# Kernel tuning notes

Measured on AMD Instinct MI355X. Metric: run time of the kernel, lower is better.

Reference implementation:

```python
import jax, jax.numpy as jnp
import numpy as np

GRID = 8        # kornia equalize_clahe default grid_size=(8,8)
NUM_BINS = 256  # kornia default
CLIP_LIMIT = 40.0


def normalize_in_range(x, lo, hi):
    mn, mx = x.min(), x.max()
    return (x - mn) / (mx - mn) * (hi - lo) + lo


def equalize_clahe(x, clip_limit=CLIP_LIMIT, grid=GRID, bins=NUM_BINS):
    # x: (B, C, H, W) in [0, 1]; H, W divisible by grid
    B, C, H, W = x.shape
    th, tw = H // grid, W // grid
    pixels = th * tw

    # --- per-pixel bin index (histc with bins=256, min=0, max=1) ---
    bidx = jnp.clip((x * bins).astype(jnp.int32), 0, bins - 1)  # (B,C,H,W)

    # --- per-tile histograms via one segment_sum (scatter-add) ---
    ti = (jnp.arange(H) // th)[None, None, :, None]
    tj = (jnp.arange(W) // tw)[None, None, None, :]
    bb = jnp.arange(B)[:, None, None, None]
    cc = jnp.arange(C)[None, :, None, None]
    tile_id = ((bb * C + cc) * grid + ti) * grid + tj          # (B,C,H,W)
    flat = (tile_id * bins + bidx).reshape(-1)
    hist = jax.ops.segment_sum(
        jnp.ones(flat.shape, jnp.float32), flat,
        num_segments=B * C * grid * grid * bins,
    ).reshape(B, C, grid, grid, bins)

    # --- clip histogram and redistribute excess uniformly ---
    max_val = max(int(clip_limit * pixels // bins), 1)
    hist = jnp.minimum(hist, max_val)
    residual = (pixels - hist.sum(-1, keepdims=True)) / bins
    hist = hist + residual

    # --- CDF -> LUT (values in [0, bins-1], floored) ---
    lut = jnp.floor(jnp.clip(jnp.cumsum(hist, axis=-1) * ((bins - 1) / pixels),
                             0.0, bins - 1.0))                 # (B,C,gh,gw,bins)

    # --- bilinear interpolation between the 4 nearest tile LUTs ---
    gi = jnp.clip((jnp.arange(H) + 0.5) / th - 0.5, 0.0, grid - 1.0)
    gj = jnp.clip((jnp.arange(W) + 0.5) / tw - 0.5, 0.0, grid - 1.0)
    i0 = jnp.floor(gi).astype(jnp.int32); i1 = jnp.minimum(i0 + 1, grid - 1)
    j0 = jnp.floor(gj).astype(jnp.int32); j1 = jnp.minimum(j0 + 1, grid - 1)
    wy = (gi - i0)[None, None, :, None]
    wx = (gj - j0)[None, None, None, :]

    I0 = i0[None, None, :, None]; I1 = i1[None, None, :, None]
    J0 = j0[None, None, None, :]; J1 = j1[None, None, None, :]

    v00 = lut[bb, cc, I0, J0, bidx]
    v01 = lut[bb, cc, I0, J1, bidx]
    v10 = lut[bb, cc, I1, J0, bidx]
    v11 = lut[bb, cc, I1, J1, bidx]

    out = (1.0 - wy) * ((1.0 - wx) * v00 + wx * v01) + wy * ((1.0 - wx) * v10 + wx * v11)
    return out / (bins - 1)


def setup_inputs() -> dict:
    key = jax.random.key(0)
    kx, ky = jax.random.split(key)
    x = jax.random.normal(kx, (16, 1, 1024, 1024), dtype=jnp.float32)
    y = jax.random.randint(ky, (16,), 0, 10, dtype=jnp.int64)
    return {"x": x, "y": y}


def reference(x, y):
    x = normalize_in_range(x, 0.0, 1.0)
    mean = x.mean(axis=(0, 2, 3))
    std = jnp.std(x, axis=(0, 2, 3), ddof=1)  # torch unbiased std
    x = (x - mean[None, :, None, None]) / std[None, :, None, None]
    x = normalize_in_range(x, 0.0, 1.0)
    x = equalize_clahe(x, clip_limit=40.0)
    return (x, y)
```

## Files before the change

kernel.cpp:

```cpp
#include <hip/hip_runtime.h>


#define BINS 256
#define FBINS 2048
#define MAXV 2560u

__global__ __launch_bounds__(256, 4) void k_tilestat(const float* __restrict__ x,
                                                     float2* __restrict__ partials,
                                                     unsigned* __restrict__ finehg){
  __shared__ unsigned fh[FBINS];
  __shared__ float smin[4], smax[4];
  __shared__ float sp[2];
  int t = threadIdx.x;
  int tile = blockIdx.x;
  int bc = tile >> 6, ti = (tile >> 3) & 7, tj = tile & 7;
  const float4* x4 = (const float4*)(x + ((size_t)bc * 1024 + ti * 128) * 1024 + tj * 128);
  float4 v[16];
  #pragma unroll
  for (int k = 0; k < 16; k++){
    int p = t + (k << 8);
    v[k] = x4[(p >> 5) * 256 + (p & 31)];
  }
  #pragma unroll
  for (int i = 0; i < FBINS / 256; i++) fh[t + i * 256] = 0u;
  float lmin = INFINITY, lmax = -INFINITY;
  #pragma unroll
  for (int k = 0; k < 16; k++){
    lmin = fminf(lmin, fminf(fminf(v[k].x, v[k].y), fminf(v[k].z, v[k].w)));
    lmax = fmaxf(lmax, fmaxf(fmaxf(v[k].x, v[k].y), fmaxf(v[k].z, v[k].w)));
  }
  for (int o = 32; o > 0; o >>= 1){
    lmin = fminf(lmin, __shfl_down(lmin, o, 64));
    lmax = fmaxf(lmax, __shfl_down(lmax, o, 64));
  }
  int lane = t & 63, wv = t >> 6;
  if (lane == 0){ smin[wv] = lmin; smax[wv] = lmax; }
  __syncthreads();
  if (t == 0){
    float m = smin[0], M = smax[0];
    #pragma unroll
    for (int i = 1; i < 4; i++){ m = fminf(m, smin[i]); M = fmaxf(M, smax[i]); }
    partials[tile] = make_float2(m, M);
    sp[0] = m;
    sp[1] = (float)FBINS / fmaxf(M - m, 1e-30f);
  }
  __syncthreads();
  float tmn = sp[0], tinv = sp[1];
  #pragma unroll
  for (int k = 0; k < 16; k++){
    int b0 = min((int)((v[k].x - tmn) * tinv), FBINS - 1);
    int b1 = min((int)((v[k].y - tmn) * tinv), FBINS - 1);
    int b2 = min((int)((v[k].z - tmn) * tinv), FBINS - 1);
    int b3 = min((int)((v[k].w - tmn) * tinv), FBINS - 1);
    atomicAdd(&fh[b0], 1u);
    atomicAdd(&fh[b1], 1u);
    atomicAdd(&fh[b2], 1u);
    atomicAdd(&fh[b3], 1u);
  }
  __syncthreads();
  unsigned* outp = finehg + (size_t)tile * (FBINS / 2);
  #pragma unroll
  for (int i = 0; i < FBINS / 512; i++){
    int w = t + i * 256;
    outp[w] = (fh[2 * w] & 0xFFFFu) | (fh[2 * w + 1] << 16);
  }
}

__global__ __launch_bounds__(256) void k_lut(const float2* __restrict__ partials,
                                             int nparts,
                                             const unsigned* __restrict__ finehg,
                                             float* __restrict__ lut,
                                             float2* __restrict__ gmm,
                                             const int* __restrict__ y,
                                             float* __restrict__ out,
                                             int N, int tail){
  __shared__ unsigned ch[BINS];
  __shared__ unsigned sc[BINS];
  __shared__ unsigned wsum[4];
  __shared__ float smin[4], smax[4];
  __shared__ float sp[2];
  int t = threadIdx.x;
  int tile = blockIdx.x;
  ch[t] = 0u;
  float lmin = INFINITY, lmax = -INFINITY;
  for (int i = t; i < nparts; i += 256){
    float2 p = partials[i];
    lmin = fminf(lmin, p.x);
    lmax = fmaxf(lmax, p.y);
  }
  for (int o = 32; o > 0; o >>= 1){
    lmin = fminf(lmin, __shfl_down(lmin, o, 64));
    lmax = fmaxf(lmax, __shfl_down(lmax, o, 64));
  }
  int lane = t & 63, wv = t >> 6;
  if (lane == 0){ smin[wv] = lmin; smax[wv] = lmax; }
  __syncthreads();
  if (t == 0){
    float m = smin[0], M = smax[0];
    #pragma unroll
    for (int i = 1; i < 4; i++){ m = fminf(m, smin[i]); M = fmaxf(M, smax[i]); }
    sp[0] = m;
    sp[1] = 1.0f / (M - m);
  }
  __syncthreads();
  float mn = sp[0], inv = sp[1];
  float2 tp = partials[tile];
  float tw = (tp.y - tp.x) * (1.0f / (float)FBINS);
  const unsigned* fhp = finehg + (size_t)tile * (FBINS / 2);
  #pragma unroll
  for (int i = 0; i < 4; i++){
    int w = t + i * 256;
    unsigned pk = fhp[w];
    unsigned c0 = pk & 0xFFFFu, c1 = pk >> 16;
    int f0 = 2 * w;
    if (c0){
      float ctr = tp.x + ((float)f0 + 0.5f) * tw;
      int cb = min(max((int)(((ctr - mn) * inv) * 256.0f), 0), 255);
      atomicAdd(&ch[cb], c0);
    }
    if (c1){
      float ctr = tp.x + ((float)f0 + 1.5f) * tw;
      int cb = min(max((int)(((ctr - mn) * inv) * 256.0f), 0), 255);
      atomicAdd(&ch[cb], c1);
    }
  }
  __syncthreads();
  unsigned h = ch[t];
  if (h > MAXV) h = MAXV;
  unsigned s = h;
  for (int o = 32; o > 0; o >>= 1) s += __shfl_down(s, o, 64);
  if (lane == 0) wsum[wv] = s;
  __syncthreads();
  unsigned total = wsum[0] + wsum[1] + wsum[2] + wsum[3];
  float residual = (16384.0f - (float)total) * (1.0f / 256.0f);
  sc[t] = h;
  __syncthreads();
  for (int o = 1; o < 256; o <<= 1){
    unsigned pv = (t >= o) ? sc[t - o] : 0u;
    __syncthreads();
    sc[t] += pv;
    __syncthreads();
  }
  float cum = ((float)sc[t] + (float)(t + 1) * residual) * (255.0f / 16384.0f);
  lut[(size_t)tile * BINS + t] = floorf(fminf(fmaxf(cum, 0.0f), 255.0f));
  if (tile == 0){
    if (t == 0) *gmm = make_float2(mn, inv);
    if (t < tail) out[N + t] = (float)y[t];
  }
}

__global__ __launch_bounds__(256) void k_apply(const float* __restrict__ x,
                                               const float2* __restrict__ gmm,
                                               const float* __restrict__ lutg,
                                               float* __restrict__ out){
  __shared__ float2 lint[2048];
  int t = threadIdx.x;
  int strip = blockIdx.x;
  int b = strip >> 7;
  int r0 = (strip & 127) << 3;
  float gi = fminf(fmaxf((r0 + 0.5f) * (1.0f / 128.0f) - 0.5f, 0.0f), 7.0f);
  int i0 = (int)gi;
  int i1 = min(i0 + 1, 7);
  const float* g0 = lutg + ((size_t)b * 8 + i0) * 2048;
  const float* g1 = lutg + ((size_t)b * 8 + i1) * 2048;
  #pragma unroll
  for (int i = 0; i < 8; i++){
    int k = t + i * 256;
    lint[k] = make_float2(g0[k], g1[k]);
  }
  float2 mmv = *gmm;
  float mn = mmv.x, inv = mmv.y;
  int j0[4], j1[4];
  float wx[4];
  #pragma unroll
  for (int c = 0; c < 4; c++){
    int col = (t << 2) + c;
    float gj = fminf(fmaxf((col + 0.5f) * (1.0f / 128.0f) - 0.5f, 0.0f), 7.0f);
    j0[c] = (int)gj;
    j1[c] = min(j0[c] + 1, 7);
    wx[c] = gj - (float)j0[c];
  }
  size_t base4 = ((size_t)b * 1024 + r0) * 256;
  __syncthreads();
  #pragma unroll
  for (int r = 0; r < 8; r++){
    int h = r0 + r;
    float giw = fminf(fmaxf((h + 0.5f) * (1.0f / 128.0f) - 0.5f, 0.0f), 7.0f);
    float wy = giw - (float)i0;
    float4 xv = ((const float4*)x)[base4 + r * 256 + t];
    int bi[4];
    bi[0] = min(max((int)(((xv.x - mn) * inv) * 256.0f), 0), 255);
    bi[1] = min(max((int)(((xv.y - mn) * inv) * 256.0f), 0), 255);
    bi[2] = min(max((int)(((xv.z - mn) * inv) * 256.0f), 0), 255);
    bi[3] = min(max((int)(((xv.w - mn) * inv) * 256.0f), 0), 255);
    float res[4];
    #pragma unroll
    for (int c = 0; c < 4; c++){
      float2 p0 = lint[(j0[c] << 8) + bi[c]];
      float2 p1 = lint[(j1[c] << 8) + bi[c]];
      float top = p0.x + wx[c] * (p1.x - p0.x);
      float bot = p0.y + wx[c] * (p1.y - p0.y);
      res[c] = (top + wy * (bot - top)) * (1.0f / 255.0f);
    }
    ((float4*)out)[base4 + r * 256 + t] = make_float4(res[0], res[1], res[2], res[3]);
  }
}

extern "C" void kernel_launch(void* const* d_in, const int* in_sizes, int n_in,
                              void* d_out, int out_size, void* d_ws, size_t ws_size,
                              hipStream_t stream){
  const float* x = (const float*)d_in[0];
  const int* y = (const int*)d_in[1];
  float* out = (float*)d_out;
  int N = in_sizes[0];
  int B = N >> 20;
  int T = B * 64;
  float2* partials = (float2*)d_ws;
  float2* gmm = (float2*)((char*)d_ws + 8192);
  unsigned* fineh = (unsigned*)((char*)d_ws + 16384);
  float* lut = (float*)((char*)d_ws + 16384 + (size_t)T * (FBINS * 2));
  int tail = out_size - N;

  hipLaunchKernelGGL(k_tilestat, dim3(T), dim3(256), 0, stream, x, partials, fineh);
  hipLaunchKernelGGL(k_lut, dim3(T), dim3(256), 0, stream,
                     partials, T, fineh, lut, gmm, y, out, N, tail);
  hipLaunchKernelGGL(k_apply, dim3(B * 128), dim3(256), 0, stream,
                     x, gmm, lut, out);
}
```

Baseline: 131.6 us.

## Fuse tile stats and LUT build into one cooperative kernel with grid sync

Merges the tile min/max pass and the LUT construction into a single cooperative kernel. Each block keeps its tile in registers, a grid-wide sync publishes the global min/max, and the block then bins directly into the final 256-bin histogram. This drops the fine 2048-bin histogram round trip through global memory and one kernel launch. The block scan is also changed to wavefront shuffles. In exchange it depends on all 1024 blocks being co-resident for the cooperative launch, and falls back to the old two-kernel path if that launch fails.

```diff
diff --git a/kernel.cpp b/kernel.cpp
--- a/kernel.cpp
+++ b/kernel.cpp
@@ -1,9 +1,112 @@
 #include <hip/hip_runtime.h>
+#include <hip/hip_cooperative_groups.h>
+
+namespace cg = cooperative_groups;
 
 
 #define BINS 256
 #define FBINS 2048
 #define MAXV 2560u
+
+__global__ __launch_bounds__(256, 4) void k_histlut(const float* __restrict__ x,
+                                                    float2* __restrict__ partials,
+                                                    float* __restrict__ lut,
+                                                    float2* __restrict__ gmm,
+                                                    const int* __restrict__ y,
+                                                    float* __restrict__ out,
+                                                    int N, int tail, int nparts){
+  __shared__ unsigned ch[BINS];
+  __shared__ float smin[4], smax[4];
+  __shared__ float sp[2];
+  __shared__ unsigned wsum[4];
+  int t = threadIdx.x;
+  int tile = blockIdx.x;
+  int bc = tile >> 6, ti = (tile >> 3) & 7, tj = tile & 7;
+  const float4* x4 = (const float4*)(x + ((size_t)bc * 1024 + ti * 128) * 1024 + tj * 128);
+  float4 v[16];
+  #pragma unroll
+  for (int k = 0; k < 16; k++){
+    int p = t + (k << 8);
+    v[k] = x4[(p >> 5) * 256 + (p & 31)];
+  }
+  ch[t] = 0u;
+  float lmin = INFINITY, lmax = -INFINITY;
+  #pragma unroll
+  for (int k = 0; k < 16; k++){
+    lmin = fminf(lmin, fminf(fminf(v[k].x, v[k].y), fminf(v[k].z, v[k].w)));
+    lmax = fmaxf(lmax, fmaxf(fmaxf(v[k].x, v[k].y), fmaxf(v[k].z, v[k].w)));
+  }
+  for (int o = 32; o > 0; o >>= 1){
+    lmin = fminf(lmin, __shfl_down(lmin, o, 64));
+    lmax = fmaxf(lmax, __shfl_down(lmax, o, 64));
+  }
+  int lane = t & 63, wv = t >> 6;
+  if (lane == 0){ smin[wv] = lmin; smax[wv] = lmax; }
+  __syncthreads();
+  if (t == 0){
+    float m = smin[0], M = smax[0];
+    #pragma unroll
+    for (int i = 1; i < 4; i++){ m = fminf(m, smin[i]); M = fmaxf(M, smax[i]); }
+    partials[tile] = make_float2(m, M);
+    __threadfence();
+  }
+  cg::this_grid().sync();
+  float gmn = INFINITY, gmx = -INFINITY;
+  for (int i = t; i < nparts; i += 256){
+    float2 p = partials[i];
+    gmn = fminf(gmn, p.x);
+    gmx = fmaxf(gmx, p.y);
+  }
+  for (int o = 32; o > 0; o >>= 1){
+    gmn = fminf(gmn, __shfl_down(gmn, o, 64));
+    gmx = fmaxf(gmx, __shfl_down(gmx, o, 64));
+  }
+  if (lane == 0){ smin[wv] = gmn; smax[wv] = gmx; }
+  __syncthreads();
+  if (t == 0){
+    float m = smin[0], M = smax[0];
+    #pragma unroll
+    for (int i = 1; i < 4; i++){ m = fminf(m, smin[i]); M = fmaxf(M, smax[i]); }
+    sp[0] = m;
+    sp[1] = 1.0f / (M - m);
+  }
+  __syncthreads();
+  float mn = sp[0], inv = sp[1];
+  #pragma unroll
+  for (int k = 0; k < 16; k++){
+    int b0 = min(max((int)(((v[k].x - mn) * inv) * 256.0f), 0), 255);
+    int b1 = min(max((int)(((v[k].y - mn) * inv) * 256.0f), 0), 255);
+    int b2 = min(max((int)(((v[k].z - mn) * inv) * 256.0f), 0), 255);
+    int b3 = min(max((int)(((v[k].w - mn) * inv) * 256.0f), 0), 255);
+    atomicAdd(&ch[b0], 1u);
+    atomicAdd(&ch[b1], 1u);
+    atomicAdd(&ch[b2], 1u);
+    atomicAdd(&ch[b3], 1u);
+  }
+  __syncthreads();
+  unsigned h = ch[t];
+  if (h > MAXV) h = MAXV;
+  unsigned s = h;
+  #pragma unroll
+  for (int o = 1; o < 64; o <<= 1){
+    unsigned nb = __shfl_up(s, o, 64);
+    if (lane >= o) s += nb;
+  }
+  if (lane == 63) wsum[wv] = s;
+  __syncthreads();
+  unsigned off = 0;
+  #pragma unroll
+  for (int i = 0; i < 3; i++) if (i < wv) off += wsum[i];
+  unsigned total = wsum[0] + wsum[1] + wsum[2] + wsum[3];
+  float residual = (16384.0f - (float)total) * (1.0f / 256.0f);
+  float cum = ((float)(s + off) + (float)(t + 1) * residual) * (255.0f / 16384.0f);
+  lut[(size_t)tile * BINS + t] = floorf(fminf(fmaxf(cum, 0.0f), 255.0f));
+  if (tile == 0){
+    if (t == 0) *gmm = make_float2(mn, inv);
+    if (t < tail) out[N + t] = (float)y[t];
+  }
+}
+
 
 __global__ __launch_bounds__(256, 4) void k_tilestat(const float* __restrict__ x,
                                                      float2* __restrict__ partials,
@@ -217,13 +320,20 @@
   int T = B * 64;
   float2* partials = (float2*)d_ws;
   float2* gmm = (float2*)((char*)d_ws + 8192);
-  unsigned* fineh = (unsigned*)((char*)d_ws + 16384);
-  float* lut = (float*)((char*)d_ws + 16384 + (size_t)T * (FBINS * 2));
+  float* lut = (float*)((char*)d_ws + 16384);
+  unsigned* fineh = (unsigned*)((char*)d_ws + (2u << 20));
   int tail = out_size - N;
 
-  hipLaunchKernelGGL(k_tilestat, dim3(T), dim3(256), 0, stream, x, partials, fineh);
-  hipLaunchKernelGGL(k_lut, dim3(T), dim3(256), 0, stream,
-                     partials, T, fineh, lut, gmm, y, out, N, tail);
+  void* args[] = { (void*)&x, (void*)&partials, (void*)&lut, (void*)&gmm,
+                   (void*)&y, (void*)&out, (void*)&N, (void*)&tail, (void*)&T };
+  hipError_t ce = hipLaunchCooperativeKernel((const void*)k_histlut,
+                                             dim3((unsigned)T), dim3(256),
+                                             args, 0, stream);
+  if (ce != hipSuccess){
+    hipLaunchKernelGGL(k_tilestat, dim3(T), dim3(256), 0, stream, x, partials, fineh);
+    hipLaunchKernelGGL(k_lut, dim3(T), dim3(256), 0, stream,
+                       partials, T, fineh, lut, gmm, y, out, N, tail);
+  }
   hipLaunchKernelGGL(k_apply, dim3(B * 128), dim3(256), 0, stream,
                      x, gmm, lut, out);
 }
```

After: 282.9 us. 2.15x slower.

## Replace fine per-tile histogram with min/max pass plus direct coarse histogram

Applied to the files above, without the earlier changes.

Drops the 2048-bin per-tile fine histogram, whose bin centres were remapped to the global bins. A grid-stride min/max pass now runs first, and a second kernel re-reads each tile and bins pixels directly into 256 global bins, using per-wave shared histograms to cut atomic contention. The block-wide shared-memory scan becomes a shuffle-based wave scan plus cross-wave offsets, and the fine-histogram workspace is removed. This gives exact binning instead of the approximate centre remap, but reads x once more (three reads in total).

```diff
diff --git a/kernel.cpp b/kernel.cpp
--- a/kernel.cpp
+++ b/kernel.cpp
@@ -2,32 +2,20 @@
 
 
 #define BINS 256
-#define FBINS 2048
 #define MAXV 2560u
 
-__global__ __launch_bounds__(256, 4) void k_tilestat(const float* __restrict__ x,
-                                                     float2* __restrict__ partials,
-                                                     unsigned* __restrict__ finehg){
-  __shared__ unsigned fh[FBINS];
+__global__ __launch_bounds__(256, 8) void k_minmax(const float4* __restrict__ x4,
+                                                   float2* __restrict__ partials,
+                                                   int nf4){
   __shared__ float smin[4], smax[4];
-  __shared__ float sp[2];
   int t = threadIdx.x;
-  int tile = blockIdx.x;
-  int bc = tile >> 6, ti = (tile >> 3) & 7, tj = tile & 7;
-  const float4* x4 = (const float4*)(x + ((size_t)bc * 1024 + ti * 128) * 1024 + tj * 128);
-  float4 v[16];
-  #pragma unroll
-  for (int k = 0; k < 16; k++){
-    int p = t + (k << 8);
-    v[k] = x4[(p >> 5) * 256 + (p & 31)];
-  }
-  #pragma unroll
-  for (int i = 0; i < FBINS / 256; i++) fh[t + i * 256] = 0u;
+  int gid = blockIdx.x * 256 + t;
+  int stride = gridDim.x * 256;
   float lmin = INFINITY, lmax = -INFINITY;
-  #pragma unroll
-  for (int k = 0; k < 16; k++){
-    lmin = fminf(lmin, fminf(fminf(v[k].x, v[k].y), fminf(v[k].z, v[k].w)));
-    lmax = fmaxf(lmax, fmaxf(fmaxf(v[k].x, v[k].y), fmaxf(v[k].z, v[k].w)));
+  for (int i = gid; i < nf4; i += stride){
+    float4 v = x4[i];
+    lmin = fminf(lmin, fminf(fminf(v.x, v.y), fminf(v.z, v.w)));
+    lmax = fmaxf(lmax, fmaxf(fmaxf(v.x, v.y), fmaxf(v.z, v.w)));
   }
   for (int o = 32; o > 0; o >>= 1){
     lmin = fminf(lmin, __shfl_down(lmin, o, 64));
@@ -40,60 +28,37 @@
     float m = smin[0], M = smax[0];
     #pragma unroll
     for (int i = 1; i < 4; i++){ m = fminf(m, smin[i]); M = fmaxf(M, smax[i]); }
-    partials[tile] = make_float2(m, M);
-    sp[0] = m;
-    sp[1] = (float)FBINS / fmaxf(M - m, 1e-30f);
-  }
-  __syncthreads();
-  float tmn = sp[0], tinv = sp[1];
-  #pragma unroll
-  for (int k = 0; k < 16; k++){
-    int b0 = min((int)((v[k].x - tmn) * tinv), FBINS - 1);
-    int b1 = min((int)((v[k].y - tmn) * tinv), FBINS - 1);
-    int b2 = min((int)((v[k].z - tmn) * tinv), FBINS - 1);
-    int b3 = min((int)((v[k].w - tmn) * tinv), FBINS - 1);
-    atomicAdd(&fh[b0], 1u);
-    atomicAdd(&fh[b1], 1u);
-    atomicAdd(&fh[b2], 1u);
-    atomicAdd(&fh[b3], 1u);
-  }
-  __syncthreads();
-  unsigned* outp = finehg + (size_t)tile * (FBINS / 2);
-  #pragma unroll
-  for (int i = 0; i < FBINS / 512; i++){
-    int w = t + i * 256;
-    outp[w] = (fh[2 * w] & 0xFFFFu) | (fh[2 * w + 1] << 16);
+    partials[blockIdx.x] = make_float2(m, M);
   }
 }
 
-__global__ __launch_bounds__(256) void k_lut(const float2* __restrict__ partials,
-                                             int nparts,
-                                             const unsigned* __restrict__ finehg,
-                                             float* __restrict__ lut,
-                                             float2* __restrict__ gmm,
-                                             const int* __restrict__ y,
-                                             float* __restrict__ out,
-                                             int N, int tail){
-  __shared__ unsigned ch[BINS];
-  __shared__ unsigned sc[BINS];
-  __shared__ unsigned wsum[4];
+__global__ __launch_bounds__(256, 4) void k_histlut(const float* __restrict__ x,
+                                                    const float2* __restrict__ partials,
+                                                    int nparts,
+                                                    float* __restrict__ lut,
+                                                    float2* __restrict__ gmm,
+                                                    const int* __restrict__ y,
+                                                    float* __restrict__ out,
+                                                    int N, int tail){
+  __shared__ unsigned hs[4][BINS];
   __shared__ float smin[4], smax[4];
   __shared__ float sp[2];
+  __shared__ unsigned wsum[4];
   int t = threadIdx.x;
   int tile = blockIdx.x;
-  ch[t] = 0u;
-  float lmin = INFINITY, lmax = -INFINITY;
+  int lane = t & 63, wv = t >> 6;
+  hs[0][t] = 0u; hs[1][t] = 0u; hs[2][t] = 0u; hs[3][t] = 0u;
+  float gmn = INFINITY, gmx = -INFINITY;
   for (int i = t; i < nparts; i += 256){
     float2 p = partials[i];
-    lmin = fminf(lmin, p.x);
-    lmax = fmaxf(lmax, p.y);
+    gmn = fminf(gmn, p.x);
+    gmx = fmaxf(gmx, p.y);
   }
   for (int o = 32; o > 0; o >>= 1){
-    lmin = fminf(lmin, __shfl_down(lmin, o, 64));
-    lmax = fmaxf(lmax, __shfl_down(lmax, o, 64));
+    gmn = fminf(gmn, __shfl_down(gmn, o, 64));
+    gmx = fmaxf(gmx, __shfl_down(gmx, o, 64));
   }
-  int lane = t & 63, wv = t >> 6;
-  if (lane == 0){ smin[wv] = lmin; smax[wv] = lmax; }
+  if (lane == 0){ smin[wv] = gmn; smax[wv] = gmx; }
   __syncthreads();
   if (t == 0){
     float m = smin[0], M = smax[0];
@@ -104,44 +69,39 @@
   }
   __syncthreads();
   float mn = sp[0], inv = sp[1];
-  float2 tp = partials[tile];
-  float tw = (tp.y - tp.x) * (1.0f / (float)FBINS);
-  const unsigned* fhp = finehg + (size_t)tile * (FBINS / 2);
+  int bc = tile >> 6, ti = (tile >> 3) & 7, tj = tile & 7;
+  const float4* x4 = (const float4*)(x + ((size_t)bc * 1024 + ti * 128) * 1024 + tj * 128);
+  unsigned* h = hs[wv];
   #pragma unroll
-  for (int i = 0; i < 4; i++){
-    int w = t + i * 256;
-    unsigned pk = fhp[w];
-    unsigned c0 = pk & 0xFFFFu, c1 = pk >> 16;
-    int f0 = 2 * w;
-    if (c0){
-      float ctr = tp.x + ((float)f0 + 0.5f) * tw;
-      int cb = min(max((int)(((ctr - mn) * inv) * 256.0f), 0), 255);
-      atomicAdd(&ch[cb], c0);
-    }
-    if (c1){
-      float ctr = tp.x + ((float)f0 + 1.5f) * tw;
-      int cb = min(max((int)(((ctr - mn) * inv) * 256.0f), 0), 255);
-      atomicAdd(&ch[cb], c1);
-    }
+  for (int k = 0; k < 16; k++){
+    int p = t + (k << 8);
+    float4 v = x4[(p >> 5) * 256 + (p & 31)];
+    int b0 = min(max((int)(((v.x - mn) * inv) * 256.0f), 0), 255);
+    int b1 = min(max((int)(((v.y - mn) * inv) * 256.0f), 0), 255);
+    int b2 = min(max((int)(((v.z - mn) * inv) * 256.0f), 0), 255);
+    int b3 = min(max((int)(((v.w - mn) * inv) * 256.0f), 0), 255);
+    atomicAdd(&h[b0], 1u);
+    atomicAdd(&h[b1], 1u);
+    atomicAdd(&h[b2], 1u);
+    atomicAdd(&h[b3], 1u);
   }
   __syncthreads();
-  unsigned h = ch[t];
-  if (h > MAXV) h = MAXV;
-  unsigned s = h;
-  for (int o = 32; o > 0; o >>= 1) s += __shfl_down(s, o, 64);
-  if (lane == 0) wsum[wv] = s;
+  unsigned hh = hs[0][t] + hs[1][t] + hs[2][t] + hs[3][t];
+  if (hh > MAXV) hh = MAXV;
+  unsigned s = hh;
+  #pragma unroll
+  for (int o = 1; o < 64; o <<= 1){
+    unsigned nb = __shfl_up(s, o, 64);
+    if (lane >= o) s += nb;
+  }
+  if (lane == 63) wsum[wv] = s;
   __syncthreads();
+  unsigned off = 0;
+  #pragma unroll
+  for (int i = 0; i < 3; i++) if (i < wv) off += wsum[i];
   unsigned total = wsum[0] + wsum[1] + wsum[2] + wsum[3];
   float residual = (16384.0f - (float)total) * (1.0f / 256.0f);
-  sc[t] = h;
-  __syncthreads();
-  for (int o = 1; o < 256; o <<= 1){
-    unsigned pv = (t >= o) ? sc[t - o] : 0u;
-    __syncthreads();
-    sc[t] += pv;
-    __syncthreads();
-  }
-  float cum = ((float)sc[t] + (float)(t + 1) * residual) * (255.0f / 16384.0f);
+  float cum = ((float)(s + off) + (float)(t + 1) * residual) * (255.0f / 16384.0f);
   lut[(size_t)tile * BINS + t] = floorf(fminf(fmaxf(cum, 0.0f), 255.0f));
   if (tile == 0){
     if (t == 0) *gmm = make_float2(mn, inv);
@@ -215,15 +175,16 @@
   int N = in_sizes[0];
   int B = N >> 20;
   int T = B * 64;
+  int nmm = B * 128;
   float2* partials = (float2*)d_ws;
-  float2* gmm = (float2*)((char*)d_ws + 8192);
-  unsigned* fineh = (unsigned*)((char*)d_ws + 16384);
-  float* lut = (float*)((char*)d_ws + 16384 + (size_t)T * (FBINS * 2));
+  float2* gmm = (float2*)((char*)d_ws + 16384);
+  float* lut = (float*)((char*)d_ws + 20480);
   int tail = out_size - N;
 
-  hipLaunchKernelGGL(k_tilestat, dim3(T), dim3(256), 0, stream, x, partials, fineh);
-  hipLaunchKernelGGL(k_lut, dim3(T), dim3(256), 0, stream,
-                     partials, T, fineh, lut, gmm, y, out, N, tail);
+  hipLaunchKernelGGL(k_minmax, dim3(nmm), dim3(256), 0, stream,
+                     (const float4*)x, partials, N >> 2);
+  hipLaunchKernelGGL(k_histlut, dim3(T), dim3(256), 0, stream,
+                     x, partials, nmm, lut, gmm, y, out, N, tail);
   hipLaunchKernelGGL(k_apply, dim3(B * 128), dim3(256), 0, stream,
                      x, gmm, lut, out);
 }
```

Result: slower. 134.4 us (+2.2%).
